# Performance work log

Hardware: AMD Instinct MI355X
Metric: run time of the kernel (lower is better)

## Reference

```python
import jax, jax.numpy as jnp
import numpy as np
import math

B, S, D, H, F = 2, 2048, 1024, 16, 4096
HD = D // H

def _xavier(key, fan_in, fan_out):
    limit = math.sqrt(6.0 / (fan_in + fan_out))
    return jax.random.uniform(key, (fan_in, fan_out), jnp.float32, -limit, limit)

def setup_inputs() -> dict:
    key = jax.random.key(0)
    ks = jax.random.split(key, 8)
    inp = {
        'x': jax.random.normal(ks[0], (B, S, D), jnp.float32),
        # attention projections (stored [in, out]; biases zero-init per module)
        'Wq': _xavier(ks[1], D, D), 'bq': jnp.zeros((D,), jnp.float32),
        'Wk': _xavier(ks[2], D, D), 'bk': jnp.zeros((D,), jnp.float32),
        'Wv': _xavier(ks[3], D, D), 'bv': jnp.zeros((D,), jnp.float32),
        'Wp': _xavier(ks[4], D, D), 'bp': jnp.zeros((D,), jnp.float32),
        # layer norms
        'g1': jnp.ones((D,), jnp.float32), 'be1': jnp.zeros((D,), jnp.float32),
        'g2': jnp.ones((D,), jnp.float32), 'be2': jnp.zeros((D,), jnp.float32),
        # feed-forward
        'W1': _xavier(ks[5], D, F), 'bf1': jnp.zeros((F,), jnp.float32),
        'W2': _xavier(ks[6], F, D), 'bf2': jnp.zeros((D,), jnp.float32),
    }
    return inp

def _layernorm(x, g, b, eps=1e-5):
    mu = jnp.mean(x, axis=-1, keepdims=True)
    var = jnp.var(x, axis=-1, keepdims=True)
    return (x - mu) * jax.lax.rsqrt(var + eps) * g + b

def _block(x, Wq, bq, Wk, bk, Wv, bv, Wp, bp, g1, be1, g2, be2, W1, bf1, W2, bf2):
    b, s, d = x.shape
    # --- pre-LN attention ---
    a_in = _layernorm(x, g1, be1)
    q = (a_in @ Wq + bq).reshape(b, s, H, HD).transpose(0, 2, 1, 3)  # [B,H,S,HD]
    k = (a_in @ Wk + bk).reshape(b, s, H, HD).transpose(0, 2, 1, 3)
    v = (a_in @ Wv + bv).reshape(b, s, H, HD).transpose(0, 2, 1, 3)
    scores = jnp.einsum('bhqd,bhkd->bhqk', q, k) / math.sqrt(HD)
    causal = jnp.tril(jnp.ones((s, s), dtype=bool))
    scores = jnp.where(causal, scores, -jnp.inf)
    attn = jax.nn.softmax(scores, axis=-1)
    out = jnp.einsum('bhqk,bhkd->bhqd', attn, v)
    out = out.transpose(0, 2, 1, 3).reshape(b, s, d)
    x = x + (out @ Wp + bp)
    # --- pre-LN feed-forward ---
    f_in = _layernorm(x, g2, be2)
    h = jax.nn.gelu(f_in @ W1 + bf1, approximate=False)
    x = x + (h @ W2 + bf2)
    return x

def reference(x, Wq, bq, Wk, bk, Wv, bv, Wp, bp, g1, be1, g2, be2, W1, bf1, W2, bf2):
    return _block(x, Wq, bq, Wk, bk, Wv, bv, Wp, bp, g1, be1, g2, be2, W1, bf1, W2, bf2)
```

## Files before the change

### kernel.cpp

```cpp
#include <hip/hip_runtime.h>
#include <hip/hip_bf16.h>

#define AS1 __attribute__((address_space(1)))
#define AS3 __attribute__((address_space(3)))

typedef __bf16 bf16;
typedef __attribute__((ext_vector_type(8))) __bf16 bf16x8;
typedef __attribute__((ext_vector_type(4))) __bf16 bf16x4;
typedef __attribute__((ext_vector_type(4))) float f32x4;

#define NB 2
#define NS 2048
#define ND 1024
#define NH 16
#define NF 4096
#define NHD 64
#define NM (NB*NS)

__device__ __forceinline__ void gload16(const void* g, void* l) {
  __builtin_amdgcn_global_load_lds((AS1 void*)g, (AS3 void*)l, 16, 0, 0);
}

__global__ void tb_pre(const float* __restrict__ x, const float* __restrict__ g1,
                       const float* __restrict__ be1, bf16* __restrict__ Abuf,
                       const float* __restrict__ Wq, const float* __restrict__ Wk,
                       const float* __restrict__ Wv, const float* __restrict__ Wp,
                       const float* __restrict__ W1, const float* __restrict__ W2,
                       bf16* __restrict__ WqT, bf16* __restrict__ WkT,
                       bf16* __restrict__ WvT, bf16* __restrict__ WpT,
                       bf16* __restrict__ W1T, bf16* __restrict__ W2T) {
  __shared__ float t[64][65];
  __shared__ float red[8];
  const int bid = blockIdx.x;
  const int tid = threadIdx.x;
  if (bid >= 3072) {
    const int row = bid - 3072;
    const float4 v = ((const float4*)(x + (size_t)row * ND))[tid];
    float s  = v.x + v.y + v.z + v.w;
    float ss = v.x*v.x + v.y*v.y + v.z*v.z + v.w*v.w;
#pragma unroll
    for (int off = 32; off; off >>= 1) {
      s  += __shfl_xor(s,  off, 64);
      ss += __shfl_xor(ss, off, 64);
    }
    const int lane = tid & 63, wv = tid >> 6;
    if (lane == 0) { red[wv] = s; red[4 + wv] = ss; }
    __syncthreads();
    s  = red[0] + red[1] + red[2] + red[3];
    ss = red[4] + red[5] + red[6] + red[7];
    const float mu = s * (1.0f / ND);
    const float var = ss * (1.0f / ND) - mu * mu;
    const float rstd = rsqrtf(var + 1e-5f);
    const float4 gv = ((const float4*)g1)[tid];
    const float4 bv = ((const float4*)be1)[tid];
    bf16x4 o;
    o[0] = (bf16)((v.x - mu) * rstd * gv.x + bv.x);
    o[1] = (bf16)((v.y - mu) * rstd * gv.y + bv.y);
    o[2] = (bf16)((v.z - mu) * rstd * gv.z + bv.z);
    o[3] = (bf16)((v.w - mu) * rstd * gv.w + bv.w);
    ((bf16x4*)(Abuf + (size_t)row * ND))[tid] = o;
    return;
  }
  const float* W; bf16* Wt; int K, N, nb, kb;
  if (bid < 1024) {
    const int z = bid >> 8, i = bid & 255;
    K = ND; N = ND; nb = (i & 15) << 6; kb = (i >> 4) << 6;
    W  = (z == 0) ? Wq  : (z == 1) ? Wk  : (z == 2) ? Wv  : Wp;
    Wt = (z == 0) ? WqT : (z == 1) ? WkT : (z == 2) ? WvT : WpT;
  } else if (bid < 2048) {
    const int i = bid - 1024;
    K = ND; N = NF; nb = (i & 63) << 6; kb = (i >> 6) << 6;
    W = W1; Wt = W1T;
  } else {
    const int i = bid - 2048;
    K = NF; N = ND; nb = (i & 15) << 6; kb = (i >> 4) << 6;
    W = W2; Wt = W2T;
  }
#pragma unroll
  for (int i = 0; i < 16; ++i) {
    const int lin = tid + (i << 8);
    const int r = lin >> 6, c = lin & 63;
    t[r][c] = W[(size_t)(kb + r) * N + nb + c];
  }
  __syncthreads();
#pragma unroll
  for (int i = 0; i < 16; ++i) {
    const int lin = tid + (i << 8);
    const int r = lin >> 6, c = lin & 63;
    Wt[(size_t)(nb + r) * K + kb + c] = (bf16)t[c][r];
  }
}

__global__ void tb_vtrans(const bf16* __restrict__ v, bf16* __restrict__ vt) {
  __shared__ bf16 t[64][72];
  const int bh = blockIdx.y;
  const int sb = blockIdx.x << 6;
  const int tid = threadIdx.x;
  const bf16* src = v + ((size_t)bh * NS + sb) * NHD;
  bf16* dst = vt + (size_t)bh * NHD * NS + sb;
  const int r = tid >> 3;
  const int c8 = (tid & 7) << 3;
#pragma unroll
  for (int i = 0; i < 2; ++i) {
    const int row = r + i * 32;
    const bf16x8 xv = *(const bf16x8*)(src + (size_t)row * NHD + c8);
#pragma unroll
    for (int j = 0; j < 8; ++j) t[row][c8 + j] = xv[j];
  }
  __syncthreads();
#pragma unroll
  for (int i = 0; i < 2; ++i) {
    const int row = r + i * 32;
    bf16x8 ov;
#pragma unroll
    for (int j = 0; j < 8; ++j) ov[j] = t[c8 + j][row];
    *(bf16x8*)(dst + (size_t)row * NS + c8) = ov;
  }
}

__global__ void tb_lnorm(const float* __restrict__ xin, const float* __restrict__ g,
                         const float* __restrict__ be, bf16* __restrict__ outp) {
  const int row = blockIdx.x;
  const int tid = threadIdx.x;
  const float4 v = ((const float4*)(xin + (size_t)row * ND))[tid];
  float s  = v.x + v.y + v.z + v.w;
  float ss = v.x*v.x + v.y*v.y + v.z*v.z + v.w*v.w;
#pragma unroll
  for (int off = 32; off; off >>= 1) {
    s  += __shfl_xor(s,  off, 64);
    ss += __shfl_xor(ss, off, 64);
  }
  __shared__ float red[8];
  const int lane = tid & 63, wv = tid >> 6;
  if (lane == 0) { red[wv] = s; red[4 + wv] = ss; }
  __syncthreads();
  s  = red[0] + red[1] + red[2] + red[3];
  ss = red[4] + red[5] + red[6] + red[7];
  const float mu = s * (1.0f / ND);
  const float var = ss * (1.0f / ND) - mu * mu;
  const float rstd = rsqrtf(var + 1e-5f);
  const float4 gv = ((const float4*)g)[tid];
  const float4 bv = ((const float4*)be)[tid];
  bf16x4 o;
  o[0] = (bf16)((v.x - mu) * rstd * gv.x + bv.x);
  o[1] = (bf16)((v.y - mu) * rstd * gv.y + bv.y);
  o[2] = (bf16)((v.z - mu) * rstd * gv.z + bv.z);
  o[3] = (bf16)((v.w - mu) * rstd * gv.w + bv.w);
  ((bf16x4*)(outp + (size_t)row * ND))[tid] = o;
}

template <int MODE>
__global__ void __launch_bounds__(256, 2)
tb_gemm(const bf16* __restrict__ A,
        const bf16* __restrict__ B0, const bf16* __restrict__ B1, const bf16* __restrict__ B2,
        const float* __restrict__ bias0, const float* __restrict__ bias1, const float* __restrict__ bias2,
        void* __restrict__ o0, void* __restrict__ o1, void* __restrict__ o2,
        int Ktot) {
  __shared__ __align__(16) bf16 As[128 * 64];
  __shared__ __align__(16) bf16 Bs[128 * 64];
  const bf16* Bt = B0; const float* bias = bias0; void* outp = o0;
  if (MODE == 0) {
    if (blockIdx.z == 1)      { Bt = B1; bias = bias1; outp = o1; }
    else if (blockIdx.z == 2) { Bt = B2; bias = bias2; outp = o2; }
  }
  const int tid = threadIdx.x;
  const int lane = tid & 63, wv = tid >> 6;
  const int wr = wv >> 1, wc = wv & 1;
  const int m0 = blockIdx.y * 128, n0 = blockIdx.x * 128;

  f32x4 acc[4][4] = {};

  const int srow = (wv << 3) + (lane >> 3);
  const int scb  = ((lane & 7) << 4);

  for (int k0 = 0; k0 < Ktot; k0 += 64) {
    __syncthreads();
#pragma unroll
    for (int i = 0; i < 4; ++i) {
      const int row = i * 32 + srow;
      const int cb = scb ^ ((row & 7) << 4);
      gload16(A  + (size_t)(m0 + row) * Ktot + k0 + (cb >> 1), (char*)As + i * 4096 + wv * 1024);
      gload16(Bt + (size_t)(n0 + row) * Ktot + k0 + (cb >> 1), (char*)Bs + i * 4096 + wv * 1024);
    }
    __syncthreads();
#pragma unroll
    for (int kk = 0; kk < 2; ++kk) {
      bf16x8 af[4], bfr[4];
#pragma unroll
      for (int mi = 0; mi < 4; ++mi) {
        const int row = wr * 64 + mi * 16 + (lane & 15);
        const int cb = (kk * 64 + ((lane >> 4) << 4)) ^ ((row & 7) << 4);
        af[mi] = *(const bf16x8*)((const char*)As + row * 128 + cb);
      }
#pragma unroll
      for (int ni = 0; ni < 4; ++ni) {
        const int row = wc * 64 + ni * 16 + (lane & 15);
        const int cb = (kk * 64 + ((lane >> 4) << 4)) ^ ((row & 7) << 4);
        bfr[ni] = *(const bf16x8*)((const char*)Bs + row * 128 + cb);
      }
#pragma unroll
      for (int mi = 0; mi < 4; ++mi)
#pragma unroll
        for (int ni = 0; ni < 4; ++ni)
          acc[mi][ni] = __builtin_amdgcn_mfma_f32_16x16x32_bf16(af[mi], bfr[ni], acc[mi][ni], 0, 0, 0);
    }
  }
  const float scale = (MODE == 0 && blockIdx.z == 0) ? 0.125f : 1.0f;
#pragma unroll
  for (int mi = 0; mi < 4; ++mi) {
#pragma unroll
    for (int ni = 0; ni < 4; ++ni) {
      const int rbase = m0 + wr * 64 + mi * 16 + ((lane >> 4) << 2);
      const int gcol  = n0 + wc * 64 + ni * 16 + (lane & 15);
#pragma unroll
      for (int r = 0; r < 4; ++r) {
        const int grow = rbase + r;
        const float val = (acc[mi][ni][r] + bias[gcol]) * scale;
        if (MODE == 0) {
          const int b = grow >> 11, sIdx = grow & 2047;
          const int h = gcol >> 6, hd = gcol & 63;
          ((bf16*)outp)[(((size_t)(b * NH + h)) * NS + sIdx) * NHD + hd] = (bf16)val;
        } else {
          const float gelu = 0.5f * val * (1.0f + erff(val * 0.70710678f));
          ((bf16*)outp)[(size_t)grow * NF + gcol] = (bf16)gelu;
        }
      }
    }
  }
}

__global__ void __launch_bounds__(256, 2)
tb_gemm64(const bf16* __restrict__ A, const bf16* __restrict__ Bt,
          const float* __restrict__ bias, const float* __restrict__ resid,
          float* __restrict__ outp, int Ktot) {
  __shared__ __align__(16) bf16 As[2][64 * 64];
  __shared__ __align__(16) bf16 Bs[2][128 * 64];
  const int bid = blockIdx.x;
  const int xcd = bid & 7, j = bid >> 3;
  const int m0 = (xcd * 8 + (j & 7)) * 64;
  const int n0 = (j >> 3) * 128;
  const int tid = threadIdx.x;
  const int lane = tid & 63, wv = tid >> 6;
  const int wr = wv >> 1, wc = wv & 1;

  f32x4 acc[2][4] = {};

  const int srow = (wv << 3) + (lane >> 3);
  const int scb  = ((lane & 7) << 4);
  const int NT = Ktot >> 6;

#define GSTAGE64(buf, t_) do {                                                 \
    _Pragma("unroll")                                                          \
    for (int i_ = 0; i_ < 2; ++i_) {                                           \
      const int row_ = i_ * 32 + srow;                                         \
      const int cb_ = scb ^ ((row_ & 7) << 4);                                 \
      gload16(A + (size_t)(m0 + row_) * Ktot + ((t_) << 6) + (cb_ >> 1),       \
              (char*)As[buf] + i_ * 4096 + wv * 1024);                         \
    }                                                                          \
    _Pragma("unroll")                                                          \
    for (int i_ = 0; i_ < 4; ++i_) {                                           \
      const int row_ = i_ * 32 + srow;                                         \
      const int cb_ = scb ^ ((row_ & 7) << 4);                                 \
      gload16(Bt + (size_t)(n0 + row_) * Ktot + ((t_) << 6) + (cb_ >> 1),      \
              (char*)Bs[buf] + i_ * 4096 + wv * 1024);                         \
    } } while (0)

  GSTAGE64(0, 0);
  asm volatile("s_waitcnt vmcnt(0)" ::: "memory");
  __builtin_amdgcn_s_barrier();

  for (int t = 0; t < NT; ++t) {
    const int cur = t & 1;
    if (t + 1 < NT) GSTAGE64(cur ^ 1, t + 1);
    const char* Ab = (const char*)As[cur];
    const char* Bb = (const char*)Bs[cur];
#pragma unroll
    for (int kk = 0; kk < 2; ++kk) {
      bf16x8 af[2], bfr[4];
#pragma unroll
      for (int mi = 0; mi < 2; ++mi) {
        const int row = wr * 32 + mi * 16 + (lane & 15);
        const int cb = (kk * 64 + ((lane >> 4) << 4)) ^ ((row & 7) << 4);
        af[mi] = *(const bf16x8*)(Ab + row * 128 + cb);
      }
#pragma unroll
      for (int ni = 0; ni < 4; ++ni) {
        const int row = wc * 64 + ni * 16 + (lane & 15);
        const int cb = (kk * 64 + ((lane >> 4) << 4)) ^ ((row & 7) << 4);
        bfr[ni] = *(const bf16x8*)(Bb + row * 128 + cb);
      }
#pragma unroll
      for (int mi = 0; mi < 2; ++mi)
#pragma unroll
        for (int ni = 0; ni < 4; ++ni)
          acc[mi][ni] = __builtin_amdgcn_mfma_f32_16x16x32_bf16(af[mi], bfr[ni], acc[mi][ni], 0, 0, 0);
    }
    if (t + 1 < NT) {
      asm volatile("s_waitcnt vmcnt(0)" ::: "memory");
      __builtin_amdgcn_s_barrier();
    }
  }
#undef GSTAGE64

#pragma unroll
  for (int mi = 0; mi < 2; ++mi) {
#pragma unroll
    for (int ni = 0; ni < 4; ++ni) {
      const int rbase = m0 + wr * 32 + mi * 16 + ((lane >> 4) << 2);
      const int gcol  = n0 + wc * 64 + ni * 16 + (lane & 15);
#pragma unroll
      for (int r = 0; r < 4; ++r) {
        const size_t idx = (size_t)(rbase + r) * ND + gcol;
        outp[idx] = resid[idx] + acc[mi][ni][r] + bias[gcol];
      }
    }
  }
}

__global__ void __launch_bounds__(256, 4)
tb_attn(const bf16* __restrict__ qg, const bf16* __restrict__ kg,
        const bf16* __restrict__ vtg, bf16* __restrict__ og) {
  __shared__ __align__(16) bf16 Ks[2][64 * 64];
  __shared__ __align__(16) bf16 Vts[2][64 * 64];
  __shared__ __align__(16) bf16 Ps[4][16 * 64];
  const int bid = blockIdx.x;
  const int u = bid & 255, v = bid >> 8;
  const int bh = u & 31;
  const int s = ((u >> 5) << 2) + v;
  const int qt = (s & 1) ? (31 - (s >> 1)) : (s >> 1);
  const int tid = threadIdx.x;
  const int lane = tid & 63, wv = tid >> 6;
  const bf16* Qp  = qg  + (size_t)bh * NS * NHD;
  const bf16* Kp  = kg  + (size_t)bh * NS * NHD;
  const bf16* Vtp = vtg + (size_t)bh * NHD * NS;
  char* const Pw = (char*)&Ps[wv][0];
  const int qbase = qt * 64 + wv * 16;

  bf16x8 qa[2];
#pragma unroll
  for (int kk = 0; kk < 2; ++kk)
    qa[kk] = *(const bf16x8*)(Qp + (size_t)(qbase + (lane & 15)) * NHD
                              + kk * 32 + ((lane >> 4) << 3));

  f32x4 Of[4] = {};
  float mrow[4], lrow[4];
#pragma unroll
  for (int r = 0; r < 4; ++r) { mrow[r] = -1e30f; lrow[r] = 0.0f; }

  const int srow = (wv << 3) + (lane >> 3);
  const int scb  = (lane & 7) << 4;
  const int nkb = qt + 1;

#define STAGE_KV(buf, kbi_) do {                                               \
    _Pragma("unroll")                                                          \
    for (int i_ = 0; i_ < 2; ++i_) {                                           \
      const int row_ = i_ * 32 + srow;                                         \
      const int cb_ = scb ^ ((row_ & 7) << 4);                                 \
      gload16(Kp  + (size_t)((kbi_) * 64 + row_) * NHD + (cb_ >> 1),           \
              (char*)Ks[buf] + i_ * 4096 + wv * 1024);                         \
      gload16(Vtp + (size_t)row_ * NS + (kbi_) * 64 + (cb_ >> 1),              \
              (char*)Vts[buf] + i_ * 4096 + wv * 1024);                        \
    } } while (0)

  STAGE_KV(0, 0);
  __syncthreads();

  for (int kbi = 0; kbi < nkb; ++kbi) {
    const int cur = kbi & 1;
    if (kbi + 1 < nkb) STAGE_KV(cur ^ 1, kbi + 1);
    const bool maskedT = (kbi == qt);

    f32x4 sf[4] = {};
#pragma unroll
    for (int kk = 0; kk < 2; ++kk) {
#pragma unroll
      for (int f = 0; f < 4; ++f) {
        const int row = f * 16 + (lane & 15);
        const int cb = (kk * 64 + ((lane >> 4) << 4)) ^ ((row & 7) << 4);
        const bf16x8 kf = *(const bf16x8*)((const char*)Ks[cur] + row * 128 + cb);
        sf[f] = __builtin_amdgcn_mfma_f32_16x16x32_bf16(qa[kk], kf, sf[f], 0, 0, 0);
      }
    }

    float tmax[4];
#pragma unroll
    for (int r = 0; r < 4; ++r) tmax[r] = -1e30f;
#pragma unroll
    for (int f = 0; f < 4; ++f)
#pragma unroll
      for (int r = 0; r < 4; ++r) {
        float sv = sf[f][r];
        if (maskedT) {
          const int kcol = kbi * 64 + f * 16 + (lane & 15);
          const int qrow = qbase + ((lane >> 4) << 2) + r;
          sv = (kcol <= qrow) ? sv : -1e30f;
          sf[f][r] = sv;
        }
        tmax[r] = fmaxf(tmax[r], sv);
      }
#pragma unroll
    for (int off = 8; off; off >>= 1)
#pragma unroll
      for (int r = 0; r < 4; ++r)
        tmax[r] = fmaxf(tmax[r], __shfl_xor(tmax[r], off, 64));
#pragma unroll
    for (int r = 0; r < 4; ++r) {
      const float mnew = fmaxf(mrow[r], tmax[r]);
      const float alpha = __expf(mrow[r] - mnew);
      mrow[r] = mnew;
      float ps = 0.0f;
#pragma unroll
      for (int f = 0; f < 4; ++f) {
        const float p = __expf(sf[f][r] - mnew);
        sf[f][r] = p;
        ps += p;
      }
      lrow[r] = lrow[r] * alpha + ps;
#pragma unroll
      for (int hf = 0; hf < 4; ++hf) Of[hf][r] *= alpha;
    }

#pragma unroll
    for (int f = 0; f < 4; ++f) {
      const int col = f * 16 + (lane & 15);
#pragma unroll
      for (int r = 0; r < 4; ++r) {
        const int prow = ((lane >> 4) << 2) + r;
        *(bf16*)(Pw + prow * 128 + ((col * 2) ^ ((prow & 7) << 4))) = (bf16)sf[f][r];
      }
    }

#pragma unroll
    for (int kk = 0; kk < 2; ++kk) {
      const int prow = lane & 15;
      const int pcb = (kk * 64 + ((lane >> 4) << 4)) ^ ((prow & 7) << 4);
      const bf16x8 pa = *(const bf16x8*)(Pw + prow * 128 + pcb);
#pragma unroll
      for (int hf = 0; hf < 4; ++hf) {
        const int vrow = hf * 16 + (lane & 15);
        const int vcb = (kk * 64 + ((lane >> 4) << 4)) ^ ((vrow & 7) << 4);
        const bf16x8 vbf = *(const bf16x8*)((const char*)Vts[cur] + vrow * 128 + vcb);
        Of[hf] = __builtin_amdgcn_mfma_f32_16x16x32_bf16(pa, vbf, Of[hf], 0, 0, 0);
      }
    }
    __syncthreads();
  }
#undef STAGE_KV

#pragma unroll
  for (int off = 8; off; off >>= 1)
#pragma unroll
    for (int r = 0; r < 4; ++r)
      lrow[r] += __shfl_xor(lrow[r], off, 64);
  const int b = bh >> 4, h = bh & 15;
#pragma unroll
  for (int r = 0; r < 4; ++r) {
    const float inv = 1.0f / lrow[r];
    const int q = qbase + ((lane >> 4) << 2) + r;
    bf16* dst = og + ((size_t)b * NS + q) * ND + h * NHD;
#pragma unroll
    for (int hf = 0; hf < 4; ++hf)
      dst[hf * 16 + (lane & 15)] = (bf16)(Of[hf][r] * inv);
  }
}

extern "C" void kernel_launch(void* const* d_in, const int* in_sizes, int n_in,
                              void* d_out, int out_size, void* d_ws, size_t ws_size,
                              hipStream_t stream) {
  (void)in_sizes; (void)n_in; (void)out_size; (void)ws_size;
  const float* x   = (const float*)d_in[0];
  const float* Wq  = (const float*)d_in[1];
  const float* bq  = (const float*)d_in[2];
  const float* Wk  = (const float*)d_in[3];
  const float* bk  = (const float*)d_in[4];
  const float* Wv  = (const float*)d_in[5];
  const float* bv  = (const float*)d_in[6];
  const float* Wp  = (const float*)d_in[7];
  const float* bp  = (const float*)d_in[8];
  const float* g1  = (const float*)d_in[9];
  const float* be1 = (const float*)d_in[10];
  const float* g2  = (const float*)d_in[11];
  const float* be2 = (const float*)d_in[12];
  const float* W1  = (const float*)d_in[13];
  const float* bf1 = (const float*)d_in[14];
  const float* W2  = (const float*)d_in[15];
  const float* bf2 = (const float*)d_in[16];
  float* outp = (float*)d_out;

  char* w = (char*)d_ws;
  bf16* WqT  = (bf16*)(w + (0u  << 20));
  bf16* WkT  = (bf16*)(w + (2u  << 20));
  bf16* WvT  = (bf16*)(w + (4u  << 20));
  bf16* WpT  = (bf16*)(w + (6u  << 20));
  bf16* W1T  = (bf16*)(w + (8u  << 20));
  bf16* W2T  = (bf16*)(w + (16u << 20));
  bf16* Abuf = (bf16*)(w + (24u << 20));
  bf16* vt   = (bf16*)(w + (24u << 20));
  bf16* qb   = (bf16*)(w + (32u << 20));
  bf16* kb   = (bf16*)(w + (40u << 20));
  bf16* vb   = (bf16*)(w + (48u << 20));
  bf16* ao   = (bf16*)(w + (56u << 20));
  bf16* hb   = (bf16*)(w + (32u << 20));
  float* x2  = outp;

  tb_pre<<<7168, 256, 0, stream>>>(x, g1, be1, Abuf, Wq, Wk, Wv, Wp, W1, W2,
                                   WqT, WkT, WvT, WpT, W1T, W2T);
  tb_gemm<0><<<dim3(8, 32, 3), 256, 0, stream>>>(Abuf, WqT, WkT, WvT, bq, bk, bv,
                                                 qb, kb, vb, ND);
  tb_vtrans<<<dim3(32, 32), 256, 0, stream>>>(vb, vt);
  tb_attn<<<1024, 256, 0, stream>>>(qb, kb, vt, ao);
  tb_gemm64<<<512, 256, 0, stream>>>(ao, WpT, bp, x, x2, ND);
  tb_lnorm<<<NM, 256, 0, stream>>>(x2, g2, be2, Abuf);
  tb_gemm<2><<<dim3(32, 32, 1), 256, 0, stream>>>(Abuf, W1T, W1T, W1T, bf1, bf1, bf1,
                                                  hb, hb, hb, ND);
  tb_gemm64<<<512, 256, 0, stream>>>(hb, W2T, bf2, x2, outp, NF);
}
```

Baseline: 246.3 us.

## Double attention query tile to 128 rows with two MFMA row groups per wave

Each attention block now processes 128 queries (32 per wave, split into two 16-row MFMA groups) instead of 64, so each staged K/V tile in LDS feeds twice as many queries. This aims to cut K/V global loads and LDS staging per query and amortize the softmax bookkeeping. The grid is halved to 512 blocks with a paired causal tile mapping, and launch bounds drop to 2 waves-groups per CU, trading occupancy and parallelism for higher per-wave register use.

```diff
diff --git a/kernel.cpp b/kernel.cpp
--- a/kernel.cpp
+++ b/kernel.cpp
@@ -317,39 +317,42 @@
   }
 }
 
-__global__ void __launch_bounds__(256, 4)
+__global__ void __launch_bounds__(256, 2)
 tb_attn(const bf16* __restrict__ qg, const bf16* __restrict__ kg,
         const bf16* __restrict__ vtg, bf16* __restrict__ og) {
   __shared__ __align__(16) bf16 Ks[2][64 * 64];
   __shared__ __align__(16) bf16 Vts[2][64 * 64];
-  __shared__ __align__(16) bf16 Ps[4][16 * 64];
+  __shared__ __align__(16) bf16 Ps[4][32 * 64];
   const int bid = blockIdx.x;
-  const int u = bid & 255, v = bid >> 8;
-  const int bh = u & 31;
-  const int s = ((u >> 5) << 2) + v;
-  const int qt = (s & 1) ? (31 - (s >> 1)) : (s >> 1);
+  const int bh = bid & 31;
+  const int s = (bid >> 5) & 7;
+  const int qt = (bid >> 8) ? (15 - s) : s;
   const int tid = threadIdx.x;
   const int lane = tid & 63, wv = tid >> 6;
   const bf16* Qp  = qg  + (size_t)bh * NS * NHD;
   const bf16* Kp  = kg  + (size_t)bh * NS * NHD;
   const bf16* Vtp = vtg + (size_t)bh * NHD * NS;
   char* const Pw = (char*)&Ps[wv][0];
-  const int qbase = qt * 64 + wv * 16;
-
-  bf16x8 qa[2];
-#pragma unroll
-  for (int kk = 0; kk < 2; ++kk)
-    qa[kk] = *(const bf16x8*)(Qp + (size_t)(qbase + (lane & 15)) * NHD
-                              + kk * 32 + ((lane >> 4) << 3));
-
-  f32x4 Of[4] = {};
-  float mrow[4], lrow[4];
-#pragma unroll
-  for (int r = 0; r < 4; ++r) { mrow[r] = -1e30f; lrow[r] = 0.0f; }
+  const int qbase = qt * 128 + wv * 32;
+
+  bf16x8 qa[2][2];
+#pragma unroll
+  for (int mi = 0; mi < 2; ++mi)
+#pragma unroll
+    for (int kk = 0; kk < 2; ++kk)
+      qa[mi][kk] = *(const bf16x8*)(Qp + (size_t)(qbase + mi * 16 + (lane & 15)) * NHD
+                                    + kk * 32 + ((lane >> 4) << 3));
+
+  f32x4 Of[2][4] = {};
+  float mrow[2][4], lrow[2][4];
+#pragma unroll
+  for (int mi = 0; mi < 2; ++mi)
+#pragma unroll
+    for (int r = 0; r < 4; ++r) { mrow[mi][r] = -1e30f; lrow[mi][r] = 0.0f; }
 
   const int srow = (wv << 3) + (lane >> 3);
   const int scb  = (lane & 7) << 4;
-  const int nkb = qt + 1;
+  const int nkb = 2 * qt + 2;
 
 #define STAGE_KV(buf, kbi_) do {                                               \
     _Pragma("unroll")                                                          \
@@ -368,9 +371,9 @@
   for (int kbi = 0; kbi < nkb; ++kbi) {
     const int cur = kbi & 1;
     if (kbi + 1 < nkb) STAGE_KV(cur ^ 1, kbi + 1);
-    const bool maskedT = (kbi == qt);
-
-    f32x4 sf[4] = {};
+    const bool maskedT = (kbi >= 2 * qt);
+
+    f32x4 sf[2][4] = {};
 #pragma unroll
     for (int kk = 0; kk < 2; ++kk) {
 #pragma unroll
@@ -378,69 +381,87 @@
         const int row = f * 16 + (lane & 15);
         const int cb = (kk * 64 + ((lane >> 4) << 4)) ^ ((row & 7) << 4);
         const bf16x8 kf = *(const bf16x8*)((const char*)Ks[cur] + row * 128 + cb);
-        sf[f] = __builtin_amdgcn_mfma_f32_16x16x32_bf16(qa[kk], kf, sf[f], 0, 0, 0);
-      }
-    }
-
-    float tmax[4];
-#pragma unroll
-    for (int r = 0; r < 4; ++r) tmax[r] = -1e30f;
-#pragma unroll
-    for (int f = 0; f < 4; ++f)
+#pragma unroll
+        for (int mi = 0; mi < 2; ++mi)
+          sf[mi][f] = __builtin_amdgcn_mfma_f32_16x16x32_bf16(qa[mi][kk], kf, sf[mi][f], 0, 0, 0);
+      }
+    }
+
+    float tmax[2][4];
+#pragma unroll
+    for (int mi = 0; mi < 2; ++mi)
+#pragma unroll
+      for (int r = 0; r < 4; ++r) tmax[mi][r] = -1e30f;
+#pragma unroll
+    for (int mi = 0; mi < 2; ++mi)
+#pragma unroll
+      for (int f = 0; f < 4; ++f)
+#pragma unroll
+        for (int r = 0; r < 4; ++r) {
+          float sv = sf[mi][f][r];
+          if (maskedT) {
+            const int kcol = kbi * 64 + f * 16 + (lane & 15);
+            const int qrow = qbase + mi * 16 + ((lane >> 4) << 2) + r;
+            sv = (kcol <= qrow) ? sv : -1e30f;
+            sf[mi][f][r] = sv;
+          }
+          tmax[mi][r] = fmaxf(tmax[mi][r], sv);
+        }
+#pragma unroll
+    for (int off = 8; off; off >>= 1)
+#pragma unroll
+      for (int mi = 0; mi < 2; ++mi)
+#pragma unroll
+        for (int r = 0; r < 4; ++r)
+          tmax[mi][r] = fmaxf(tmax[mi][r], __shfl_xor(tmax[mi][r], off, 64));
+#pragma unroll
+    for (int mi = 0; mi < 2; ++mi)
 #pragma unroll
       for (int r = 0; r < 4; ++r) {
-        float sv = sf[f][r];
-        if (maskedT) {
-          const int kcol = kbi * 64 + f * 16 + (lane & 15);
-          const int qrow = qbase + ((lane >> 4) << 2) + r;
-          sv = (kcol <= qrow) ? sv : -1e30f;
-          sf[f][r] = sv;
+        const float mnew = fmaxf(mrow[mi][r], tmax[mi][r]);
+        const float alpha = __expf(mrow[mi][r] - mnew);
+        mrow[mi][r] = mnew;
+        float ps = 0.0f;
+#pragma unroll
+        for (int f = 0; f < 4; ++f) {
+          const float p = __expf(sf[mi][f][r] - mnew);
+          sf[mi][f][r] = p;
+          ps += p;
         }
-        tmax[r] = fmaxf(tmax[r], sv);
-      }
-#pragma unroll
-    for (int off = 8; off; off >>= 1)
-#pragma unroll
-      for (int r = 0; r < 4; ++r)
-        tmax[r] = fmaxf(tmax[r], __shfl_xor(tmax[r], off, 64));
-#pragma unroll
-    for (int r = 0; r < 4; ++r) {
-      const float mnew = fmaxf(mrow[r], tmax[r]);
-      const float alpha = __expf(mrow[r] - mnew);
-      mrow[r] = mnew;
-      float ps = 0.0f;
+        lrow[mi][r] = lrow[mi][r] * alpha + ps;
+#pragma unroll
+        for (int hf = 0; hf < 4; ++hf) Of[mi][hf][r] *= alpha;
+      }
+
+#pragma unroll
+    for (int mi = 0; mi < 2; ++mi)
 #pragma unroll
       for (int f = 0; f < 4; ++f) {
-        const float p = __expf(sf[f][r] - mnew);
-        sf[f][r] = p;
-        ps += p;
-      }
-      lrow[r] = lrow[r] * alpha + ps;
-#pragma unroll
-      for (int hf = 0; hf < 4; ++hf) Of[hf][r] *= alpha;
-    }
-
-#pragma unroll
-    for (int f = 0; f < 4; ++f) {
-      const int col = f * 16 + (lane & 15);
-#pragma unroll
-      for (int r = 0; r < 4; ++r) {
-        const int prow = ((lane >> 4) << 2) + r;
-        *(bf16*)(Pw + prow * 128 + ((col * 2) ^ ((prow & 7) << 4))) = (bf16)sf[f][r];
-      }
-    }
+        const int col = f * 16 + (lane & 15);
+#pragma unroll
+        for (int r = 0; r < 4; ++r) {
+          const int prow = mi * 16 + ((lane >> 4) << 2) + r;
+          *(bf16*)(Pw + prow * 128 + ((col * 2) ^ ((prow & 7) << 4))) = (bf16)sf[mi][f][r];
+        }
+      }
 
 #pragma unroll
     for (int kk = 0; kk < 2; ++kk) {
-      const int prow = lane & 15;
-      const int pcb = (kk * 64 + ((lane >> 4) << 4)) ^ ((prow & 7) << 4);
-      const bf16x8 pa = *(const bf16x8*)(Pw + prow * 128 + pcb);
+      bf16x8 pa[2];
+#pragma unroll
+      for (int mi = 0; mi < 2; ++mi) {
+        const int prow = mi * 16 + (lane & 15);
+        const int pcb = (kk * 64 + ((lane >> 4) << 4)) ^ ((prow & 7) << 4);
+        pa[mi] = *(const bf16x8*)(Pw + prow * 128 + pcb);
+      }
 #pragma unroll
       for (int hf = 0; hf < 4; ++hf) {
         const int vrow = hf * 16 + (lane & 15);
         const int vcb = (kk * 64 + ((lane >> 4) << 4)) ^ ((vrow & 7) << 4);
         const bf16x8 vbf = *(const bf16x8*)((const char*)Vts[cur] + vrow * 128 + vcb);
-        Of[hf] = __builtin_amdgcn_mfma_f32_16x16x32_bf16(pa, vbf, Of[hf], 0, 0, 0);
+#pragma unroll
+        for (int mi = 0; mi < 2; ++mi)
+          Of[mi][hf] = __builtin_amdgcn_mfma_f32_16x16x32_bf16(pa[mi], vbf, Of[mi][hf], 0, 0, 0);
       }
     }
     __syncthreads();
@@ -450,18 +471,22 @@
 #pragma unroll
   for (int off = 8; off; off >>= 1)
 #pragma unroll
-    for (int r = 0; r < 4; ++r)
-      lrow[r] += __shfl_xor(lrow[r], off, 64);
+    for (int mi = 0; mi < 2; ++mi)
+#pragma unroll
+      for (int r = 0; r < 4; ++r)
+        lrow[mi][r] += __shfl_xor(lrow[mi][r], off, 64);
   const int b = bh >> 4, h = bh & 15;
 #pragma unroll
-  for (int r = 0; r < 4; ++r) {
-    const float inv = 1.0f / lrow[r];
-    const int q = qbase + ((lane >> 4) << 2) + r;
-    bf16* dst = og + ((size_t)b * NS + q) * ND + h * NHD;
-#pragma unroll
-    for (int hf = 0; hf < 4; ++hf)
-      dst[hf * 16 + (lane & 15)] = (bf16)(Of[hf][r] * inv);
-  }
+  for (int mi = 0; mi < 2; ++mi)
+#pragma unroll
+    for (int r = 0; r < 4; ++r) {
+      const float inv = 1.0f / lrow[mi][r];
+      const int q = qbase + mi * 16 + ((lane >> 4) << 2) + r;
+      bf16* dst = og + ((size_t)b * NS + q) * ND + h * NHD;
+#pragma unroll
+      for (int hf = 0; hf < 4; ++hf)
+        dst[hf * 16 + (lane & 15)] = (bf16)(Of[mi][hf][r] * inv);
+    }
 }
 
 extern "C" void kernel_launch(void* const* d_in, const int* in_sizes, int n_in,
@@ -508,7 +533,7 @@
   tb_gemm<0><<<dim3(8, 32, 3), 256, 0, stream>>>(Abuf, WqT, WkT, WvT, bq, bk, bv,
                                                  qb, kb, vb, ND);
   tb_vtrans<<<dim3(32, 32), 256, 0, stream>>>(vb, vt);
-  tb_attn<<<1024, 256, 0, stream>>>(qb, kb, vt, ao);
+  tb_attn<<<512, 256, 0, stream>>>(qb, kb, vt, ao);
   tb_gemm64<<<512, 256, 0, stream>>>(ao, WpT, bp, x, x2, ND);
   tb_lnorm<<<NM, 256, 0, stream>>>(x2, g2, be2, Abuf);
   tb_gemm<2><<<dim3(32, 32, 1), 256, 0, stream>>>(Abuf, W1T, W1T, W1T, bf1, bf1, bf1,
```

Result: slower. 263.7 us (+7.1%).
